# Kernel tuning notes

Measured on AMD Instinct MI355X. Metric: run time of the kernel, lower is better.

The kernel has to match this reference:

```python
import jax, jax.numpy as jnp
import numpy as np

H = 16  # num heads

def setup_inputs() -> dict:
    key = jax.random.key(0)
    k1, k2, k3 = jax.random.split(key, 3)
    B, L, D = 2, 2048, 1024
    x = jax.random.normal(k1, (B, L, D), dtype=jnp.float32)
    # torch Linear weight is [out,in]; we store transposed [in,out] so y = x @ W
    w_qkv = jax.random.normal(k2, (D, 3 * D), dtype=jnp.float32) * (D ** -0.5)
    w_proj = jax.random.normal(k3, (D, D), dtype=jnp.float32) * (D ** -0.5)
    return {"x": x, "w_qkv": w_qkv, "w_proj": w_proj, "num_prefix_tokens": 256}

def _prefix_causal_mask(L: int, M: int):
    # True = masked. Strict upper triangle (causal), then text rows (M:) may
    # see ALL prefix columns (:M).
    mask = jnp.triu(jnp.ones((L, L), dtype=bool), k=1)
    mask = mask.at[M:, :M].set(False)
    return mask

def reference(x, w_qkv, w_proj, num_prefix_tokens):
    B, L, D = x.shape
    d = D // H
    scale = d ** -0.5
    qkv = (x @ w_qkv).reshape(B, L, 3, H, d)
    q = jnp.transpose(qkv[:, :, 0], (0, 2, 1, 3))  # [B,H,L,d]
    k = jnp.transpose(qkv[:, :, 1], (0, 2, 1, 3))
    v = jnp.transpose(qkv[:, :, 2], (0, 2, 1, 3))
    logits = jnp.einsum("bhqd,bhkd->bhqk", q, k) * scale  # [B,H,L,L]
    mask = _prefix_causal_mask(L, num_prefix_tokens)
    logits = jnp.where(mask[None, None], -jnp.inf, logits)
    attn = jax.nn.softmax(logits, axis=-1)
    out = jnp.einsum("bhqk,bhkd->bhqd", attn, v)  # [B,H,L,d]
    out = jnp.transpose(out, (0, 2, 1, 3)).reshape(B, L, D)
    return out @ w_proj
```

## Files before the change

kernel.cpp:

```cpp
#include <hip/hip_runtime.h>
#include <hip/hip_bf16.h>

#define BATCH   2
#define L_SEQ   2048
#define DMODEL  1024
#define NHEADS  16
#define DHEAD   64
#define SEG     (BATCH*NHEADS*L_SEQ*DHEAD)

typedef __attribute__((ext_vector_type(8)))  short bf16x8;
typedef __attribute__((ext_vector_type(4)))  float f32x4;
typedef __attribute__((ext_vector_type(16))) float f32x16;

__device__ __forceinline__ unsigned short f2b(float f) {
    unsigned int u = __float_as_uint(f);
    return (unsigned short)((u + 0x7FFFu + ((u >> 16) & 1u)) >> 16);
}
__device__ __forceinline__ unsigned int pk2(float a, float b) {
    __hip_bfloat162 h = __float22bfloat162_rn(make_float2(a, b));
    return *(unsigned int*)&h;
}
__device__ __forceinline__ void glds16(const unsigned short* g, unsigned short* l) {
    __builtin_amdgcn_global_load_lds(
        (const __attribute__((address_space(1))) unsigned int*)g,
        (__attribute__((address_space(3))) unsigned int*)l, 16, 0, 0);
}

__device__ __forceinline__ void tcast64(const float* __restrict__ in,
                                        unsigned short* __restrict__ out,
                                        int K, int N, int bx, int by, int t) {
    __shared__ unsigned short T[64][65];
    const int k0 = by * 64, n0 = bx * 64;
    const int r = t >> 4, c4 = (t & 15) * 4;
#pragma unroll
    for (int rep = 0; rep < 4; ++rep) {
        int kk = rep * 16 + r;
        float4 f = *(const float4*)&in[(size_t)(k0 + kk) * N + n0 + c4];
        T[kk][c4 + 0] = f2b(f.x);
        T[kk][c4 + 1] = f2b(f.y);
        T[kk][c4 + 2] = f2b(f.z);
        T[kk][c4 + 3] = f2b(f.w);
    }
    __syncthreads();
#pragma unroll
    for (int rep = 0; rep < 4; ++rep) {
        int nn = rep * 16 + r;
        ushort4 o;
        o.x = T[c4 + 0][nn];
        o.y = T[c4 + 1][nn];
        o.z = T[c4 + 2][nn];
        o.w = T[c4 + 3][nn];
        *(ushort4*)&out[(size_t)(n0 + nn) * K + k0 + c4] = o;
    }
}

__global__ __launch_bounds__(256)
void prep(const float* __restrict__ x, const float* __restrict__ wqkv,
          const float* __restrict__ wproj, unsigned short* __restrict__ xb,
          unsigned short* __restrict__ wqkvT, unsigned short* __restrict__ wprojT) {
    const int id = blockIdx.x, t = threadIdx.x;
    if (id < 4096) {
        int i = id * 1024 + t * 4;
        float4 f = *(const float4*)&x[i];
        ushort4 o;
        o.x = f2b(f.x); o.y = f2b(f.y); o.z = f2b(f.z); o.w = f2b(f.w);
        *(ushort4*)&xb[i] = o;
    } else if (id < 4864) {
        int lid = id - 4096;
        tcast64(wqkv, wqkvT, DMODEL, 3 * DMODEL, lid % 48, lid / 48, t);
    } else {
        int lid = id - 4864;
        tcast64(wproj, wprojT, DMODEL, DMODEL, lid & 15, lid >> 4, t);
    }
}

__global__ __launch_bounds__(256)
void gemm_qkv(const unsigned short* __restrict__ A, const unsigned short* __restrict__ Bt,
              unsigned short* __restrict__ Cb) {
    __shared__ unsigned short SLDS[2 * 128 * 128];

    const int t = threadIdx.x;
    const int lane = t & 63, wave = t >> 6;
    const int quad = lane >> 4, l16 = lane & 15;
    const int wm = (wave >> 1) * 64, wn = (wave & 1) * 64;
    const int id = blockIdx.y * gridDim.x + blockIdx.x;
    const int xcd = id & 7, sq = id >> 3;
    const int m0 = (xcd * 4 + sq / 24) * 128;
    const int n0 = (sq % 24) * 128;
    const bool vrole = (n0 >= 2048);

    const int gsw = (lane & 7) ^ (lane >> 3);
    const unsigned short* ga[4];
    const unsigned short* gb[4];
    int ldA[4], ldB[4];
#pragma unroll
    for (int i = 0; i < 4; ++i) {
        int row = wave * 32 + i * 8 + (lane >> 3);
        ga[i] = &A[(size_t)(m0 + row) * DMODEL + gsw * 8];
        gb[i] = &Bt[(size_t)(n0 + row) * DMODEL + gsw * 8];
        ldA[i] = (wave * 32 + i * 8) * 64;
        ldB[i] = 8192 + (wave * 32 + i * 8) * 64;
    }
    const int sx = l16 & 7;

    f32x4 acc[4][4];
#pragma unroll
    for (int i = 0; i < 4; ++i)
#pragma unroll
        for (int j = 0; j < 4; ++j)
#pragma unroll
            for (int r = 0; r < 4; ++r) acc[i][j][r] = 0.0f;

#pragma unroll
    for (int i = 0; i < 4; ++i) {
        glds16(ga[i], &SLDS[ldA[i]]);
        glds16(gb[i], &SLDS[ldB[i]]);
    }
    __syncthreads();

    int cur = 0;
    for (int kt = 0; kt < 16; ++kt) {
        if (kt < 15) {
            const int ko = (kt + 1) * 64;
            unsigned short* dst = &SLDS[(cur ^ 1) * 16384];
#pragma unroll
            for (int i = 0; i < 4; ++i) {
                glds16(ga[i] + ko, dst + ldA[i]);
                glds16(gb[i] + ko, dst + ldB[i]);
            }
        }
        const unsigned short* Asm = &SLDS[cur * 16384];
        const unsigned short* Bsm = Asm + 8192;
#pragma unroll
        for (int s = 0; s < 2; ++s) {
            bf16x8 af[4], bfr[4];
#pragma unroll
            for (int i = 0; i < 4; ++i)
                af[i] = *(const bf16x8*)&Asm[(wm + i * 16 + l16) * 64 + ((4 * s + quad) ^ sx) * 8];
#pragma unroll
            for (int j = 0; j < 4; ++j)
                bfr[j] = *(const bf16x8*)&Bsm[(wn + j * 16 + l16) * 64 + ((4 * s + quad) ^ sx) * 8];
            __builtin_amdgcn_s_setprio(1);
            if (!vrole) {
#pragma unroll
                for (int i = 0; i < 4; ++i)
#pragma unroll
                    for (int j = 0; j < 4; ++j)
                        acc[i][j] = __builtin_amdgcn_mfma_f32_16x16x32_bf16(af[i], bfr[j], acc[i][j], 0, 0, 0);
            } else {
#pragma unroll
                for (int i = 0; i < 4; ++i)
#pragma unroll
                    for (int j = 0; j < 4; ++j)
                        acc[i][j] = __builtin_amdgcn_mfma_f32_16x16x32_bf16(bfr[j], af[i], acc[i][j], 0, 0, 0);
            }
            __builtin_amdgcn_s_setprio(0);
        }
        __syncthreads();
        cur ^= 1;
    }

    const float qscale = 0.1803368801111244f;
    const float scl = (!vrole && n0 < 1024) ? qscale : 1.0f;
#pragma unroll
    for (int i = 0; i < 4; ++i)
#pragma unroll
        for (int r = 0; r < 4; ++r) {
#pragma unroll
            for (int j = 0; j < 4; ++j) {
                int row_l, col_l;
                if (!vrole) {
                    row_l = wm + i * 16 + quad * 4 + r;
                    col_l = wn + j * 16 + l16;
                } else {
                    row_l = wn + j * 16 + quad * 4 + r;
                    col_l = wm + i * 16 + l16;
                }
                int key = row_l & 7;
                SLDS[row_l * 128 + (((col_l >> 3) ^ key) * 8) + (col_l & 7)] =
                    f2b(acc[i][j][r] * scl);
            }
        }
    __syncthreads();

    const int s0 = n0 >> 10;
    const int bb = m0 >> 11;
#pragma unroll
    for (int it = 0; it < 4; ++it) {
        int row = it * 32 + (t >> 3);
        int c = t & 7;
        int key = row & 7;
        bf16x8 v0 = *(const bf16x8*)&SLDS[row * 128 + ((c ^ key) * 8)];
        bf16x8 v1 = *(const bf16x8*)&SLDS[row * 128 + (((c + 8) ^ key) * 8)];
        if (!vrole) {
            int token = m0 + row, lp = token & (L_SEQ - 1);
            int n_a = n0 + c * 8,        h_a = (n_a >> 6) & 15, d_a = n_a & 63;
            int n_b = n0 + (c + 8) * 8,  h_b = (n_b >> 6) & 15, d_b = n_b & 63;
            size_t base = (size_t)s0 * SEG;
            *(bf16x8*)&Cb[base + (((size_t)(bb * NHEADS + h_a) * L_SEQ + lp) * DHEAD) + d_a] = v0;
            *(bf16x8*)&Cb[base + (((size_t)(bb * NHEADS + h_b) * L_SEQ + lp) * DHEAD) + d_b] = v1;
        } else {
            int fr = (n0 - 2048) + row;
            int h = fr >> 6, dd = fr & 63;
            int lp0 = (m0 & (L_SEQ - 1));
            size_t base = 2 * (size_t)SEG +
                          (((size_t)(bb * NHEADS + h) * DHEAD + dd) * L_SEQ) + lp0;
            *(bf16x8*)&Cb[base + c * 8]       = v0;
            *(bf16x8*)&Cb[base + (c + 8) * 8] = v1;
        }
    }
}

__global__ __launch_bounds__(256)
void gemm_proj(const unsigned short* __restrict__ A, const unsigned short* __restrict__ Bt,
               float* __restrict__ Cf) {
    __shared__ unsigned short SLDS[2 * 128 * 128];

    const int t = threadIdx.x;
    const int lane = t & 63, wave = t >> 6;
    const int quad = lane >> 4, l16 = lane & 15;
    const int wm = (wave >> 1) * 64, wn = (wave & 1) * 64;
    const int id = blockIdx.y * gridDim.x + blockIdx.x;
    const int xcd = id & 7, sq = id >> 3;
    const int m0 = (xcd * 4 + (sq >> 3)) * 128;
    const int n0 = (sq & 7) * 128;

    const int gsw = (lane & 7) ^ (lane >> 3);
    const unsigned short* ga[4];
    const unsigned short* gb[4];
    int ldA[4], ldB[4];
#pragma unroll
    for (int i = 0; i < 4; ++i) {
        int row = wave * 32 + i * 8 + (lane >> 3);
        ga[i] = &A[(size_t)(m0 + row) * DMODEL + gsw * 8];
        gb[i] = &Bt[(size_t)(n0 + row) * DMODEL + gsw * 8];
        ldA[i] = (wave * 32 + i * 8) * 64;
        ldB[i] = 8192 + (wave * 32 + i * 8) * 64;
    }
    const int sx = l16 & 7;

    f32x4 acc[4][4];
#pragma unroll
    for (int i = 0; i < 4; ++i)
#pragma unroll
        for (int j = 0; j < 4; ++j)
#pragma unroll
            for (int r = 0; r < 4; ++r) acc[i][j][r] = 0.0f;

#pragma unroll
    for (int i = 0; i < 4; ++i) {
        glds16(ga[i], &SLDS[ldA[i]]);
        glds16(gb[i], &SLDS[ldB[i]]);
    }
    __syncthreads();

    int cur = 0;
    for (int kt = 0; kt < 16; ++kt) {
        if (kt < 15) {
            const int ko = (kt + 1) * 64;
            unsigned short* dst = &SLDS[(cur ^ 1) * 16384];
#pragma unroll
            for (int i = 0; i < 4; ++i) {
                glds16(ga[i] + ko, dst + ldA[i]);
                glds16(gb[i] + ko, dst + ldB[i]);
            }
        }
        const unsigned short* Asm = &SLDS[cur * 16384];
        const unsigned short* Bsm = Asm + 8192;
#pragma unroll
        for (int s = 0; s < 2; ++s) {
            bf16x8 af[4], bfr[4];
#pragma unroll
            for (int i = 0; i < 4; ++i)
                af[i] = *(const bf16x8*)&Asm[(wm + i * 16 + l16) * 64 + ((4 * s + quad) ^ sx) * 8];
#pragma unroll
            for (int j = 0; j < 4; ++j)
                bfr[j] = *(const bf16x8*)&Bsm[(wn + j * 16 + l16) * 64 + ((4 * s + quad) ^ sx) * 8];
            __builtin_amdgcn_s_setprio(1);
#pragma unroll
            for (int i = 0; i < 4; ++i)
#pragma unroll
                for (int j = 0; j < 4; ++j)
                    acc[i][j] = __builtin_amdgcn_mfma_f32_16x16x32_bf16(af[i], bfr[j], acc[i][j], 0, 0, 0);
            __builtin_amdgcn_s_setprio(0);
        }
        __syncthreads();
        cur ^= 1;
    }

#pragma unroll
    for (int i = 0; i < 4; ++i)
#pragma unroll
        for (int r = 0; r < 4; ++r) {
            int row = m0 + wm + i * 16 + quad * 4 + r;
#pragma unroll
            for (int j = 0; j < 4; ++j)
                Cf[(size_t)row * DMODEL + n0 + wn + j * 16 + l16] = acc[i][j][r];
        }
}

__global__ __launch_bounds__(256)
void attn_mfma(const unsigned short* __restrict__ Qg, const unsigned short* __restrict__ Kg,
               const unsigned short* __restrict__ Vg, unsigned short* __restrict__ Ao) {
    __shared__ unsigned short Ksm[128 * 64];
    __shared__ unsigned short Vsm[64 * 128];
    __shared__ unsigned short Psm[4 * 32 * 64];

    const int t = threadIdx.x;
    const int lane = t & 63, wave = t >> 6;
    const int l31 = lane & 31, hi = lane >> 5;
    const int bh = blockIdx.x & 31;
    const int Qt = 31 - (blockIdx.x >> 5);
    const int q0 = Qt * 64;
    const int qh = wave & 1, kp = wave >> 1;
    const int wq0 = q0 + qh * 32;
    const int nstrip = (Qt >> 1) + 1;
    const int b = bh >> 4, h = bh & 15;
    const size_t qkbase = (size_t)bh * L_SEQ * DHEAD;
    const size_t vbase  = (size_t)bh * DHEAD * L_SEQ;

    bf16x8 bq[4];
#pragma unroll
    for (int ks = 0; ks < 4; ++ks)
        bq[ks] = *(const bf16x8*)&Qg[qkbase + (size_t)(wq0 + l31) * DHEAD + ks * 16 + hi * 8];

    const int kc0 = t & 7,  kr0 = (t >> 3) * 4;
    const int vc0 = t & 15, vd0 = (t >> 4) * 4;

    unsigned short* Pw = Psm + wave * 32 * 64;

    f32x16 O0, O1;
#pragma unroll
    for (int r = 0; r < 16; ++r) { O0[r] = 0.0f; O1[r] = 0.0f; }
    float rs = 0.0f;

    bf16x8 gk[4], gv[4];
#pragma unroll
    for (int i = 0; i < 4; ++i) {
        gk[i] = *(const bf16x8*)&Kg[qkbase + (size_t)(kr0 + i) * DHEAD + kc0 * 8];
        gv[i] = *(const bf16x8*)&Vg[vbase + (size_t)(vd0 + i) * L_SEQ + vc0 * 8];
    }

    for (int s = 0; s < nstrip; ++s) {
        __syncthreads();
#pragma unroll
        for (int i = 0; i < 4; ++i) {
            *(bf16x8*)&Ksm[(kc0 * 128 + ((kr0 + i) ^ kc0)) * 8] = gk[i];
            *(bf16x8*)&Vsm[(vc0 * 64 + ((vd0 + i) ^ vc0)) * 8] = gv[i];
        }
        if (s + 1 < nstrip) {
            const int kn = (s + 1) * 128;
#pragma unroll
            for (int i = 0; i < 4; ++i) {
                gk[i] = *(const bf16x8*)&Kg[qkbase + (size_t)(kn + kr0 + i) * DHEAD + kc0 * 8];
                gv[i] = *(const bf16x8*)&Vg[vbase + (size_t)(vd0 + i) * L_SEQ + kn + vc0 * 8];
            }
        }
        __syncthreads();

        const int keybase = s * 128 + kp * 64;
        if (keybase <= wq0 + 31) {
            f32x16 ST[2];
            __builtin_amdgcn_s_setprio(1);
#pragma unroll
            for (int kh = 0; kh < 2; ++kh) {
#pragma unroll
                for (int r = 0; r < 16; ++r) ST[kh][r] = 0.0f;
#pragma unroll
                for (int ks = 0; ks < 4; ++ks) {
                    const int c = ks * 2 + hi;
                    const int rk = kp * 64 + kh * 32 + l31;
                    bf16x8 a = *(const bf16x8*)&Ksm[(c * 128 + (rk ^ c)) * 8];
                    ST[kh] = __builtin_amdgcn_mfma_f32_32x32x16_bf16(a, bq[ks], ST[kh], 0, 0, 0);
                }
            }
            __builtin_amdgcn_s_setprio(0);

            if (keybase + 63 > wq0) {
                const int qg = wq0 + l31;
#pragma unroll
                for (int kh = 0; kh < 2; ++kh)
#pragma unroll
                    for (int r = 0; r < 16; ++r) {
                        int keyg = keybase + kh * 32 + (r & 3) + 8 * (r >> 2) + 4 * hi;
                        if (keyg > qg) ST[kh][r] = -1e30f;
                    }
            }

#pragma unroll
            for (int kh = 0; kh < 2; ++kh)
#pragma unroll
                for (int g = 0; g < 4; ++g) {
                    float p0 = __builtin_amdgcn_exp2f(ST[kh][4 * g + 0]);
                    float p1 = __builtin_amdgcn_exp2f(ST[kh][4 * g + 1]);
                    float p2 = __builtin_amdgcn_exp2f(ST[kh][4 * g + 2]);
                    float p3 = __builtin_amdgcn_exp2f(ST[kh][4 * g + 3]);
                    rs += (p0 + p1) + (p2 + p3);
                    const int c = kh * 4 + g;
                    *(uint2*)&Pw[(c * 32 + (l31 ^ c)) * 8 + hi * 4] =
                        make_uint2(pk2(p0, p1), pk2(p2, p3));
                }

            __builtin_amdgcn_s_setprio(1);
#pragma unroll
            for (int ks = 0; ks < 4; ++ks) {
                const int cp = ks * 2 + hi;
                const int cv = kp * 8 + ks * 2 + hi;
                bf16x8 pa = *(const bf16x8*)&Pw[(cp * 32 + (l31 ^ cp)) * 8];
                bf16x8 v0 = *(const bf16x8*)&Vsm[(cv * 64 + (l31 ^ cv)) * 8];
                bf16x8 v1 = *(const bf16x8*)&Vsm[(cv * 64 + ((32 + l31) ^ cv)) * 8];
                O0 = __builtin_amdgcn_mfma_f32_32x32x16_bf16(pa, v0, O0, 0, 0, 0);
                O1 = __builtin_amdgcn_mfma_f32_32x32x16_bf16(pa, v1, O1, 0, 0, 0);
            }
            __builtin_amdgcn_s_setprio(0);
        }
    }

    rs += __shfl_xor(rs, 32, 64);

    __syncthreads();
    float* Oex = (float*)Ksm;
    float* Rex = (float*)Vsm;
    if (kp == 1) {
#pragma unroll
        for (int r = 0; r < 16; ++r) {
            int qloc = (r & 3) + 8 * (r >> 2) + 4 * hi;
            Oex[qh * 2048 + qloc * 64 + l31]      = O0[r];
            Oex[qh * 2048 + qloc * 64 + 32 + l31] = O1[r];
        }
        if (hi == 0) Rex[qh * 32 + l31] = rs;
    }
    __syncthreads();
    if (kp == 0) {
        float rs_tot = rs + Rex[qh * 32 + l31];
        float linv = 1.0f / rs_tot;
        float lf[16];
#pragma unroll
        for (int r = 0; r < 16; ++r) {
            int qloc = (r & 3) + 8 * (r >> 2) + 4 * hi;
            O0[r] += Oex[qh * 2048 + qloc * 64 + l31];
            O1[r] += Oex[qh * 2048 + qloc * 64 + 32 + l31];
            lf[r] = __shfl(linv, qloc, 32);
        }
#pragma unroll
        for (int r = 0; r < 16; ++r) {
            int qloc = (r & 3) + 8 * (r >> 2) + 4 * hi;
            int token = wq0 + qloc;
            size_t ob = ((size_t)(b * L_SEQ + token)) * DMODEL + h * DHEAD;
            Ao[ob + l31]      = f2b(O0[r] * lf[r]);
            Ao[ob + 32 + l31] = f2b(O1[r] * lf[r]);
        }
    }
}

extern "C" void kernel_launch(void* const* d_in, const int* in_sizes, int n_in,
                              void* d_out, int out_size, void* d_ws, size_t ws_size,
                              hipStream_t stream) {
    const float* x      = (const float*)d_in[0];
    const float* w_qkv  = (const float*)d_in[1];
    const float* w_proj = (const float*)d_in[2];
    float* out = (float*)d_out;

    unsigned short* ws     = (unsigned short*)d_ws;
    unsigned short* xb     = ws;
    unsigned short* wqkvT  = xb + 4194304;
    unsigned short* wprojT = wqkvT + 3145728;
    unsigned short* qkv    = wprojT + 1048576;
    unsigned short* ao     = qkv + 3 * (size_t)SEG;

    prep<<<5120, 256, 0, stream>>>(x, w_qkv, w_proj, xb, wqkvT, wprojT);

    gemm_qkv<<<dim3(24, 32), 256, 0, stream>>>(xb, wqkvT, qkv);

    attn_mfma<<<1024, 256, 0, stream>>>(qkv, qkv + SEG, qkv + 2 * (size_t)SEG, ao);

    gemm_proj<<<dim3(8, 32), 256, 0, stream>>>(ao, wprojT, out);
}
```

Measured before the change: 176.6 us.

## Split each 128-key strip across four waves per query half in attention

Doubles the attention block to 512 threads, so each 128-key strip is divided among four key-partition waves of 32 keys each instead of two waves of 64. Each wave does half the QK and PV MFMA work per strip, and the K/V staging loads per thread are halved. The partial outputs and row sums from three partner waves are reduced through shared memory at the end. In exchange it uses more LDS, adds a larger final reduction, and raises register pressure per block, which may lower occupancy.

```diff
diff --git a/kernel.cpp b/kernel.cpp
--- a/kernel.cpp
+++ b/kernel.cpp
@@ -299,12 +299,14 @@
         }
 }
 
-__global__ __launch_bounds__(256)
+__global__ __launch_bounds__(512)
 void attn_mfma(const unsigned short* __restrict__ Qg, const unsigned short* __restrict__ Kg,
                const unsigned short* __restrict__ Vg, unsigned short* __restrict__ Ao) {
-    __shared__ unsigned short Ksm[128 * 64];
-    __shared__ unsigned short Vsm[64 * 128];
-    __shared__ unsigned short Psm[4 * 32 * 64];
+    __shared__ unsigned short SLDS[24576];
+    __shared__ float Rex[192];
+    unsigned short* Ksm = SLDS;
+    unsigned short* Vsm = SLDS + 8192;
+    unsigned short* Psm = SLDS + 16384;
 
     const int t = threadIdx.x;
     const int lane = t & 63, wave = t >> 6;
@@ -324,19 +326,19 @@
     for (int ks = 0; ks < 4; ++ks)
         bq[ks] = *(const bf16x8*)&Qg[qkbase + (size_t)(wq0 + l31) * DHEAD + ks * 16 + hi * 8];
 
-    const int kc0 = t & 7,  kr0 = (t >> 3) * 4;
-    const int vc0 = t & 15, vd0 = (t >> 4) * 4;
-
-    unsigned short* Pw = Psm + wave * 32 * 64;
+    const int kc0 = t & 7,  kr0 = (t >> 3) * 2;
+    const int vc0 = t & 15, vd0 = (t >> 4) * 2;
+
+    unsigned short* Pw = Psm + wave * 1024;
 
     f32x16 O0, O1;
 #pragma unroll
     for (int r = 0; r < 16; ++r) { O0[r] = 0.0f; O1[r] = 0.0f; }
     float rs = 0.0f;
 
-    bf16x8 gk[4], gv[4];
-#pragma unroll
-    for (int i = 0; i < 4; ++i) {
+    bf16x8 gk[2], gv[2];
+#pragma unroll
+    for (int i = 0; i < 2; ++i) {
         gk[i] = *(const bf16x8*)&Kg[qkbase + (size_t)(kr0 + i) * DHEAD + kc0 * 8];
         gv[i] = *(const bf16x8*)&Vg[vbase + (size_t)(vd0 + i) * L_SEQ + vc0 * 8];
     }
@@ -344,68 +346,60 @@
     for (int s = 0; s < nstrip; ++s) {
         __syncthreads();
 #pragma unroll
-        for (int i = 0; i < 4; ++i) {
+        for (int i = 0; i < 2; ++i) {
             *(bf16x8*)&Ksm[(kc0 * 128 + ((kr0 + i) ^ kc0)) * 8] = gk[i];
             *(bf16x8*)&Vsm[(vc0 * 64 + ((vd0 + i) ^ vc0)) * 8] = gv[i];
         }
         if (s + 1 < nstrip) {
             const int kn = (s + 1) * 128;
 #pragma unroll
-            for (int i = 0; i < 4; ++i) {
+            for (int i = 0; i < 2; ++i) {
                 gk[i] = *(const bf16x8*)&Kg[qkbase + (size_t)(kn + kr0 + i) * DHEAD + kc0 * 8];
                 gv[i] = *(const bf16x8*)&Vg[vbase + (size_t)(vd0 + i) * L_SEQ + kn + vc0 * 8];
             }
         }
         __syncthreads();
 
-        const int keybase = s * 128 + kp * 64;
+        const int keybase = s * 128 + kp * 32;
         if (keybase <= wq0 + 31) {
-            f32x16 ST[2];
+            f32x16 ST;
+#pragma unroll
+            for (int r = 0; r < 16; ++r) ST[r] = 0.0f;
             __builtin_amdgcn_s_setprio(1);
 #pragma unroll
-            for (int kh = 0; kh < 2; ++kh) {
-#pragma unroll
-                for (int r = 0; r < 16; ++r) ST[kh][r] = 0.0f;
-#pragma unroll
-                for (int ks = 0; ks < 4; ++ks) {
-                    const int c = ks * 2 + hi;
-                    const int rk = kp * 64 + kh * 32 + l31;
-                    bf16x8 a = *(const bf16x8*)&Ksm[(c * 128 + (rk ^ c)) * 8];
-                    ST[kh] = __builtin_amdgcn_mfma_f32_32x32x16_bf16(a, bq[ks], ST[kh], 0, 0, 0);
+            for (int ks = 0; ks < 4; ++ks) {
+                const int c = ks * 2 + hi;
+                const int rk = kp * 32 + l31;
+                bf16x8 a = *(const bf16x8*)&Ksm[(c * 128 + (rk ^ c)) * 8];
+                ST = __builtin_amdgcn_mfma_f32_32x32x16_bf16(a, bq[ks], ST, 0, 0, 0);
+            }
+            __builtin_amdgcn_s_setprio(0);
+
+            if (keybase + 31 > wq0) {
+                const int qg = wq0 + l31;
+#pragma unroll
+                for (int r = 0; r < 16; ++r) {
+                    int keyg = keybase + (r & 3) + 8 * (r >> 2) + 4 * hi;
+                    if (keyg > qg) ST[r] = -1e30f;
                 }
             }
-            __builtin_amdgcn_s_setprio(0);
-
-            if (keybase + 63 > wq0) {
-                const int qg = wq0 + l31;
-#pragma unroll
-                for (int kh = 0; kh < 2; ++kh)
-#pragma unroll
-                    for (int r = 0; r < 16; ++r) {
-                        int keyg = keybase + kh * 32 + (r & 3) + 8 * (r >> 2) + 4 * hi;
-                        if (keyg > qg) ST[kh][r] = -1e30f;
-                    }
-            }
-
-#pragma unroll
-            for (int kh = 0; kh < 2; ++kh)
-#pragma unroll
-                for (int g = 0; g < 4; ++g) {
-                    float p0 = __builtin_amdgcn_exp2f(ST[kh][4 * g + 0]);
-                    float p1 = __builtin_amdgcn_exp2f(ST[kh][4 * g + 1]);
-                    float p2 = __builtin_amdgcn_exp2f(ST[kh][4 * g + 2]);
-                    float p3 = __builtin_amdgcn_exp2f(ST[kh][4 * g + 3]);
-                    rs += (p0 + p1) + (p2 + p3);
-                    const int c = kh * 4 + g;
-                    *(uint2*)&Pw[(c * 32 + (l31 ^ c)) * 8 + hi * 4] =
-                        make_uint2(pk2(p0, p1), pk2(p2, p3));
-                }
+
+#pragma unroll
+            for (int g = 0; g < 4; ++g) {
+                float p0 = __builtin_amdgcn_exp2f(ST[4 * g + 0]);
+                float p1 = __builtin_amdgcn_exp2f(ST[4 * g + 1]);
+                float p2 = __builtin_amdgcn_exp2f(ST[4 * g + 2]);
+                float p3 = __builtin_amdgcn_exp2f(ST[4 * g + 3]);
+                rs += (p0 + p1) + (p2 + p3);
+                *(uint2*)&Pw[(g * 32 + (l31 ^ g)) * 8 + hi * 4] =
+                    make_uint2(pk2(p0, p1), pk2(p2, p3));
+            }
 
             __builtin_amdgcn_s_setprio(1);
 #pragma unroll
-            for (int ks = 0; ks < 4; ++ks) {
+            for (int ks = 0; ks < 2; ++ks) {
                 const int cp = ks * 2 + hi;
-                const int cv = kp * 8 + ks * 2 + hi;
+                const int cv = kp * 4 + cp;
                 bf16x8 pa = *(const bf16x8*)&Pw[(cp * 32 + (l31 ^ cp)) * 8];
                 bf16x8 v0 = *(const bf16x8*)&Vsm[(cv * 64 + (l31 ^ cv)) * 8];
                 bf16x8 v1 = *(const bf16x8*)&Vsm[(cv * 64 + ((32 + l31) ^ cv)) * 8];
@@ -419,27 +413,32 @@
     rs += __shfl_xor(rs, 32, 64);
 
     __syncthreads();
-    float* Oex = (float*)Ksm;
-    float* Rex = (float*)Vsm;
-    if (kp == 1) {
+    float* Oex = (float*)SLDS;
+    if (kp != 0) {
+        const int g = (qh * 3 + (kp - 1)) * 2048;
 #pragma unroll
         for (int r = 0; r < 16; ++r) {
             int qloc = (r & 3) + 8 * (r >> 2) + 4 * hi;
-            Oex[qh * 2048 + qloc * 64 + l31]      = O0[r];
-            Oex[qh * 2048 + qloc * 64 + 32 + l31] = O1[r];
-        }
-        if (hi == 0) Rex[qh * 32 + l31] = rs;
+            Oex[g + qloc * 64 + l31]      = O0[r];
+            Oex[g + qloc * 64 + 32 + l31] = O1[r];
+        }
+        if (hi == 0) Rex[(qh * 3 + (kp - 1)) * 32 + l31] = rs;
     }
     __syncthreads();
     if (kp == 0) {
-        float rs_tot = rs + Rex[qh * 32 + l31];
+        float rs_tot = rs;
+#pragma unroll
+        for (int p = 0; p < 3; ++p) rs_tot += Rex[(qh * 3 + p) * 32 + l31];
         float linv = 1.0f / rs_tot;
         float lf[16];
 #pragma unroll
         for (int r = 0; r < 16; ++r) {
             int qloc = (r & 3) + 8 * (r >> 2) + 4 * hi;
-            O0[r] += Oex[qh * 2048 + qloc * 64 + l31];
-            O1[r] += Oex[qh * 2048 + qloc * 64 + 32 + l31];
+#pragma unroll
+            for (int p = 0; p < 3; ++p) {
+                O0[r] += Oex[(qh * 3 + p) * 2048 + qloc * 64 + l31];
+                O1[r] += Oex[(qh * 3 + p) * 2048 + qloc * 64 + 32 + l31];
+            }
             lf[r] = __shfl(linv, qloc, 32);
         }
 #pragma unroll
@@ -472,7 +471,7 @@
 
     gemm_qkv<<<dim3(24, 32), 256, 0, stream>>>(xb, wqkvT, qkv);
 
-    attn_mfma<<<1024, 256, 0, stream>>>(qkv, qkv + SEG, qkv + 2 * (size_t)SEG, ao);
+    attn_mfma<<<1024, 512, 0, stream>>>(qkv, qkv + SEG, qkv + 2 * (size_t)SEG, ao);
 
     gemm_proj<<<dim3(8, 32), 256, 0, stream>>>(ao, wprojT, out);
 }
```

New measurement: 170.0 us. 3.8% less time.

## Load K and V fragments directly from global memory into registers in attention

Applied to the files above, without the earlier changes.

The attention kernel no longer stages K and V strips through shared memory with block-wide barriers. Each wave loads its own K and V MFMA fragments straight from global (L2) memory and skips non-causal strips with an early continue. This removes the __syncthreads pairs and the LDS traffic, and shrinks shared memory so more blocks can be resident. In exchange, both key-halves' waves re-read overlapping data from global memory, the loads are less coalesced (strided rows of 16 bytes), and prefetching across strips is lost.

```diff
diff --git a/kernel.cpp b/kernel.cpp
--- a/kernel.cpp
+++ b/kernel.cpp
@@ -302,9 +302,8 @@
 __global__ __launch_bounds__(256)
 void attn_mfma(const unsigned short* __restrict__ Qg, const unsigned short* __restrict__ Kg,
                const unsigned short* __restrict__ Vg, unsigned short* __restrict__ Ao) {
-    __shared__ unsigned short Ksm[128 * 64];
-    __shared__ unsigned short Vsm[64 * 128];
     __shared__ unsigned short Psm[4 * 32 * 64];
+    __shared__ float Rex[64];
 
     const int t = threadIdx.x;
     const int lane = t & 63, wave = t >> 6;
@@ -324,103 +323,94 @@
     for (int ks = 0; ks < 4; ++ks)
         bq[ks] = *(const bf16x8*)&Qg[qkbase + (size_t)(wq0 + l31) * DHEAD + ks * 16 + hi * 8];
 
-    const int kc0 = t & 7,  kr0 = (t >> 3) * 4;
-    const int vc0 = t & 15, vd0 = (t >> 4) * 4;
-
-    unsigned short* Pw = Psm + wave * 32 * 64;
+    unsigned short* Pw = Psm + wave * 2048;
 
     f32x16 O0, O1;
 #pragma unroll
     for (int r = 0; r < 16; ++r) { O0[r] = 0.0f; O1[r] = 0.0f; }
     float rs = 0.0f;
 
-    bf16x8 gk[4], gv[4];
-#pragma unroll
-    for (int i = 0; i < 4; ++i) {
-        gk[i] = *(const bf16x8*)&Kg[qkbase + (size_t)(kr0 + i) * DHEAD + kc0 * 8];
-        gv[i] = *(const bf16x8*)&Vg[vbase + (size_t)(vd0 + i) * L_SEQ + vc0 * 8];
-    }
-
     for (int s = 0; s < nstrip; ++s) {
-        __syncthreads();
-#pragma unroll
-        for (int i = 0; i < 4; ++i) {
-            *(bf16x8*)&Ksm[(kc0 * 128 + ((kr0 + i) ^ kc0)) * 8] = gk[i];
-            *(bf16x8*)&Vsm[(vc0 * 64 + ((vd0 + i) ^ vc0)) * 8] = gv[i];
-        }
-        if (s + 1 < nstrip) {
-            const int kn = (s + 1) * 128;
-#pragma unroll
-            for (int i = 0; i < 4; ++i) {
-                gk[i] = *(const bf16x8*)&Kg[qkbase + (size_t)(kn + kr0 + i) * DHEAD + kc0 * 8];
-                gv[i] = *(const bf16x8*)&Vg[vbase + (size_t)(vd0 + i) * L_SEQ + kn + vc0 * 8];
+        const int keybase = s * 128 + kp * 64;
+        if (keybase > wq0 + 31) continue;
+
+        const unsigned short* Kst = &Kg[qkbase + (size_t)keybase * DHEAD];
+        bf16x8 kf0[4], kf1[4];
+#pragma unroll
+        for (int ks = 0; ks < 4; ++ks) {
+            const int dd = (ks * 2 + hi) * 8;
+            kf0[ks] = *(const bf16x8*)&Kst[(size_t)l31 * DHEAD + dd];
+            kf1[ks] = *(const bf16x8*)&Kst[(size_t)(32 + l31) * DHEAD + dd];
+        }
+
+        f32x16 ST0, ST1;
+#pragma unroll
+        for (int r = 0; r < 16; ++r) { ST0[r] = 0.0f; ST1[r] = 0.0f; }
+        __builtin_amdgcn_s_setprio(1);
+#pragma unroll
+        for (int ks = 0; ks < 4; ++ks)
+            ST0 = __builtin_amdgcn_mfma_f32_32x32x16_bf16(kf0[ks], bq[ks], ST0, 0, 0, 0);
+#pragma unroll
+        for (int ks = 0; ks < 4; ++ks)
+            ST1 = __builtin_amdgcn_mfma_f32_32x32x16_bf16(kf1[ks], bq[ks], ST1, 0, 0, 0);
+        __builtin_amdgcn_s_setprio(0);
+
+        const unsigned short* Vst = &Vg[vbase + keybase];
+        bf16x8 vf0[4], vf1[4];
+#pragma unroll
+        for (int ks = 0; ks < 4; ++ks) {
+            const int ko = (ks * 2 + hi) * 8;
+            vf0[ks] = *(const bf16x8*)&Vst[(size_t)l31 * L_SEQ + ko];
+            vf1[ks] = *(const bf16x8*)&Vst[(size_t)(32 + l31) * L_SEQ + ko];
+        }
+
+        if (keybase + 63 > wq0) {
+            const int qg = wq0 + l31;
+#pragma unroll
+            for (int r = 0; r < 16; ++r) {
+                int keyg = keybase + (r & 3) + 8 * (r >> 2) + 4 * hi;
+                if (keyg > qg)      ST0[r] = -1e30f;
+                if (keyg + 32 > qg) ST1[r] = -1e30f;
             }
         }
-        __syncthreads();
-
-        const int keybase = s * 128 + kp * 64;
-        if (keybase <= wq0 + 31) {
-            f32x16 ST[2];
-            __builtin_amdgcn_s_setprio(1);
-#pragma unroll
-            for (int kh = 0; kh < 2; ++kh) {
-#pragma unroll
-                for (int r = 0; r < 16; ++r) ST[kh][r] = 0.0f;
-#pragma unroll
-                for (int ks = 0; ks < 4; ++ks) {
-                    const int c = ks * 2 + hi;
-                    const int rk = kp * 64 + kh * 32 + l31;
-                    bf16x8 a = *(const bf16x8*)&Ksm[(c * 128 + (rk ^ c)) * 8];
-                    ST[kh] = __builtin_amdgcn_mfma_f32_32x32x16_bf16(a, bq[ks], ST[kh], 0, 0, 0);
-                }
-            }
-            __builtin_amdgcn_s_setprio(0);
-
-            if (keybase + 63 > wq0) {
-                const int qg = wq0 + l31;
-#pragma unroll
-                for (int kh = 0; kh < 2; ++kh)
-#pragma unroll
-                    for (int r = 0; r < 16; ++r) {
-                        int keyg = keybase + kh * 32 + (r & 3) + 8 * (r >> 2) + 4 * hi;
-                        if (keyg > qg) ST[kh][r] = -1e30f;
-                    }
-            }
-
-#pragma unroll
-            for (int kh = 0; kh < 2; ++kh)
-#pragma unroll
-                for (int g = 0; g < 4; ++g) {
-                    float p0 = __builtin_amdgcn_exp2f(ST[kh][4 * g + 0]);
-                    float p1 = __builtin_amdgcn_exp2f(ST[kh][4 * g + 1]);
-                    float p2 = __builtin_amdgcn_exp2f(ST[kh][4 * g + 2]);
-                    float p3 = __builtin_amdgcn_exp2f(ST[kh][4 * g + 3]);
-                    rs += (p0 + p1) + (p2 + p3);
-                    const int c = kh * 4 + g;
-                    *(uint2*)&Pw[(c * 32 + (l31 ^ c)) * 8 + hi * 4] =
-                        make_uint2(pk2(p0, p1), pk2(p2, p3));
-                }
-
-            __builtin_amdgcn_s_setprio(1);
-#pragma unroll
-            for (int ks = 0; ks < 4; ++ks) {
-                const int cp = ks * 2 + hi;
-                const int cv = kp * 8 + ks * 2 + hi;
-                bf16x8 pa = *(const bf16x8*)&Pw[(cp * 32 + (l31 ^ cp)) * 8];
-                bf16x8 v0 = *(const bf16x8*)&Vsm[(cv * 64 + (l31 ^ cv)) * 8];
-                bf16x8 v1 = *(const bf16x8*)&Vsm[(cv * 64 + ((32 + l31) ^ cv)) * 8];
-                O0 = __builtin_amdgcn_mfma_f32_32x32x16_bf16(pa, v0, O0, 0, 0, 0);
-                O1 = __builtin_amdgcn_mfma_f32_32x32x16_bf16(pa, v1, O1, 0, 0, 0);
-            }
-            __builtin_amdgcn_s_setprio(0);
-        }
+
+#pragma unroll
+        for (int g = 0; g < 4; ++g) {
+            float p0 = __builtin_amdgcn_exp2f(ST0[4 * g + 0]);
+            float p1 = __builtin_amdgcn_exp2f(ST0[4 * g + 1]);
+            float p2 = __builtin_amdgcn_exp2f(ST0[4 * g + 2]);
+            float p3 = __builtin_amdgcn_exp2f(ST0[4 * g + 3]);
+            rs += (p0 + p1) + (p2 + p3);
+            *(uint2*)&Pw[(g * 32 + (l31 ^ g)) * 8 + hi * 4] =
+                make_uint2(pk2(p0, p1), pk2(p2, p3));
+        }
+#pragma unroll
+        for (int g = 0; g < 4; ++g) {
+            float p0 = __builtin_amdgcn_exp2f(ST1[4 * g + 0]);
+            float p1 = __builtin_amdgcn_exp2f(ST1[4 * g + 1]);
+            float p2 = __builtin_amdgcn_exp2f(ST1[4 * g + 2]);
+            float p3 = __builtin_amdgcn_exp2f(ST1[4 * g + 3]);
+            rs += (p0 + p1) + (p2 + p3);
+            const int c = 4 + g;
+            *(uint2*)&Pw[(c * 32 + (l31 ^ c)) * 8 + hi * 4] =
+                make_uint2(pk2(p0, p1), pk2(p2, p3));
+        }
+
+        __builtin_amdgcn_s_setprio(1);
+#pragma unroll
+        for (int ks = 0; ks < 4; ++ks) {
+            const int cp = ks * 2 + hi;
+            bf16x8 pa = *(const bf16x8*)&Pw[(cp * 32 + (l31 ^ cp)) * 8];
+            O0 = __builtin_amdgcn_mfma_f32_32x32x16_bf16(pa, vf0[ks], O0, 0, 0, 0);
+            O1 = __builtin_amdgcn_mfma_f32_32x32x16_bf16(pa, vf1[ks], O1, 0, 0, 0);
+        }
+        __builtin_amdgcn_s_setprio(0);
     }
 
     rs += __shfl_xor(rs, 32, 64);
 
     __syncthreads();
-    float* Oex = (float*)Ksm;
-    float* Rex = (float*)Vsm;
+    float* Oex = (float*)Psm;
     if (kp == 1) {
 #pragma unroll
         for (int r = 0; r < 16; ++r) {
```

Result: slower. 205.9 us (+16.6%).
